# Performance work log

Hardware: AMD Instinct MI355X
Metric: run time of the kernel (lower is better)

## Reference

```python
import jax, jax.numpy as jnp
import numpy as np


def setup_inputs() -> dict:
    key = jax.random.key(0)
    ks = jax.random.split(key, 8)
    B, L, I, H, O = 512, 512, 256, 1024, 1
    def glorot(k, shape, fan_sum):
        return jax.random.uniform(k, shape, jnp.float32, -1.0, 1.0) * (6.0 / fan_sum) ** 0.5
    return {
        "X": jax.random.normal(ks[0], (B, L, I), jnp.float32),
        "W_in1": glorot(ks[1], (H, I), H + I),
        "b_in1": jnp.zeros((H, 1), jnp.float32),
        "W_rec1": glorot(ks[2], (H, H), H + H),
        "W_in2": glorot(ks[3], (H, I), H + I),
        "b_in2": jnp.zeros((H, 1), jnp.float32),
        "W_rec2": glorot(ks[4], (H, H), H + H),
        "W_out": glorot(ks[5], (O, H), O + H),
        "b_out": jnp.zeros((O, 1), jnp.float32),
    }


def reference(X, W_in1, b_in1, W_rec1, W_in2, b_in2, W_rec2, W_out, b_out):
    B, L, I = X.shape
    H = W_in1.shape[0]
    Xs = jnp.swapaxes(X, 0, 1)  # (L, B, I)
    # Precompute the input-to-hidden projections for all timesteps (parallel GEMMs).
    in1 = jnp.einsum("hi,lbi->lbh", W_in1, Xs) + b_in1[:, 0]  # (L, B, H)
    in2 = jnp.einsum("hi,lbi->lbh", W_in2, Xs) + b_in2[:, 0]  # (L, B, H)
    even = (jnp.arange(L) % 2 == 0)[:, None, None]  # (L, 1, 1) broadcast mask

    def step(carry, xs):
        z12, z1, z2 = carry  # each (B, H)
        a1, a2, ev = xs
        z1n = jnp.tanh(a1 + z12 @ W_rec1.T)
        z2n = jnp.where(ev, jnp.tanh(a2 + z2 @ W_rec2.T), z2)  # branch updates only on even l
        return (z1n + z2n, z1n, z2n), None

    z0 = jnp.zeros((B, H), X.dtype)
    (z12, z1, z2), _ = jax.lax.scan(step, (z0, z0, z0), (in1, in2, even))
    z_out = jnp.tanh(z1 @ W_out.T + b_out[:, 0])  # (B, num_outputs)
    return z_out.reshape(B, 1)
```

## Files before the change

### kernel.cpp

```cpp
#include <hip/hip_runtime.h>
#include <hip/hip_bf16.h>

typedef __attribute__((ext_vector_type(8))) short bhalf8;
typedef __attribute__((ext_vector_type(4))) float fvec4;
typedef __attribute__((ext_vector_type(4))) unsigned u32x4;

static __device__ __forceinline__ unsigned short f2bf(float f) {
  unsigned u = __builtin_bit_cast(unsigned, f);
  u = (u + 0x7fffu + ((u >> 16) & 1u)) >> 16;
  return (unsigned short)u;
}
static __device__ __forceinline__ float tanh_fast(float x) {
  x = fminf(12.f, fmaxf(-12.f, x));
  float e = __expf(2.f * x);
  return (e - 1.f) / (e + 1.f);
}
static __device__ __forceinline__ fvec4 tanh4(fvec4 v) {
  fvec4 r;
  r[0] = tanh_fast(v[0]); r[1] = tanh_fast(v[1]);
  r[2] = tanh_fast(v[2]); r[3] = tanh_fast(v[3]);
  return r;
}
static __device__ __forceinline__ bhalf8 load_w8(const float* p) {
  fvec4 a = *(const fvec4*)p;
  fvec4 b = *(const fvec4*)(p + 4);
  bhalf8 r;
  r[0] = (short)f2bf(a[0]); r[1] = (short)f2bf(a[1]);
  r[2] = (short)f2bf(a[2]); r[3] = (short)f2bf(a[3]);
  r[4] = (short)f2bf(b[0]); r[5] = (short)f2bf(b[1]);
  r[6] = (short)f2bf(b[2]); r[7] = (short)f2bf(b[3]);
  return r;
}

static __device__ __forceinline__ void st_f32_coh(float* p, float v) {
  asm volatile("global_store_dword %0, %1, off sc0 sc1" :: "v"(p), "v"(v) : "memory");
}
static __device__ __forceinline__ void st_u32_coh(unsigned* p, unsigned v) {
  asm volatile("global_store_dword %0, %1, off sc0 sc1" :: "v"(p), "v"(v) : "memory");
}
static __device__ __forceinline__ void st16_coh(void* p, u32x4 v) {
  asm volatile("global_store_dwordx4 %0, %1, off sc0 sc1" :: "v"(p), "v"(v) : "memory");
}
static __device__ __forceinline__ unsigned ld_u32_coh(const unsigned* p) {
  unsigned v;
  asm volatile("global_load_dword %0, %1, off sc0 sc1\n\ts_waitcnt vmcnt(0)"
               : "=v"(v) : "v"(p) : "memory");
  return v;
}
static __device__ __forceinline__ float ld_f32_coh(const float* p) {
  float v;
  asm volatile("global_load_dword %0, %1, off sc0 sc1\n\ts_waitcnt vmcnt(0)"
               : "=v"(v) : "v"(p) : "memory");
  return v;
}
static __device__ __forceinline__ void gll16_coh(const void* g, void* lds) {
  __builtin_amdgcn_global_load_lds(
      (const __attribute__((address_space(1))) void*)g,
      (__attribute__((address_space(3))) void*)lds, 16, 0, 0x11);
}

#define MFMA16(a, b, c) __builtin_amdgcn_mfma_f32_16x16x32_bf16((a), (b), (c), 0, 0, 0)

extern "C" __global__ void __launch_bounds__(256, 1)
alarm_rnn_persist(const float* __restrict__ X, const float* __restrict__ Win1,
                  const float* __restrict__ bin1, const float* __restrict__ Wrec1,
                  const float* __restrict__ Win2, const float* __restrict__ bin2,
                  const float* __restrict__ Wrec2, const float* __restrict__ Wout,
                  const float* __restrict__ bout, float* __restrict__ out,
                  unsigned* flags, unsigned short* gbuf0, unsigned short* gbuf1,
                  unsigned short* z2b0, unsigned short* z2b1, float* z1buf)
{
  constexpr int kL = 512, kI = 256, kH = 1024;
  extern __shared__ char smem[];

  const int tid = threadIdx.x, bid = blockIdx.x;
  const int grp = bid >> 4, memb = bid & 15;
  const int lane = tid & 63, w = tid >> 6;
  const int row16 = lane & 15, kq = lane >> 4;
  const int sw = (row16 & 7) << 4;
  const int hcol = memb * 64 + w * 16 + row16;
  const int brow0 = grp * 32;

  bhalf8 w1[32], w2[32], wi1[8], wi2[8];
  {
    const float* p1 = Wrec1 + (size_t)hcol * kH + kq * 8;
    const float* p2 = Wrec2 + (size_t)hcol * kH + kq * 8;
#pragma unroll
    for (int kk = 0; kk < 32; ++kk) {
      w1[kk] = load_w8(p1 + kk * 32);
      w2[kk] = load_w8(p2 + kk * 32);
    }
    const float* q1 = Win1 + (size_t)hcol * kI + kq * 8;
    const float* q2 = Win2 + (size_t)hcol * kI + kq * 8;
#pragma unroll
    for (int kk = 0; kk < 8; ++kk) {
      wi1[kk] = load_w8(q1 + kk * 32);
      wi2[kk] = load_w8(q2 + kk * 32);
    }
  }
  const float bv1 = bin1[hcol];
  const float bv2 = bin2[hcol];
  fvec4 z2c0 = {0.f, 0.f, 0.f, 0.f}, z2c1 = {0.f, 0.f, 0.f, 0.f};

  {
    int r = tid >> 3, q = tid & 7;
#pragma unroll
    for (int p = 0; p < 2; ++p) {
      const float* xp = X + (size_t)(brow0 + r) * (kL * kI) + (size_t)p * kI;
      fvec4 xv[8];
#pragma unroll
      for (int j = 0; j < 8; ++j) xv[j] = *(const fvec4*)(xp + q * 4 + j * 32);
#pragma unroll
      for (int j = 0; j < 8; ++j) {
        int i0 = q * 4 + j * 32;
        ushort4 pk;
        pk.x = f2bf(xv[j][0]); pk.y = f2bf(xv[j][1]);
        pk.z = f2bf(xv[j][2]); pk.w = f2bf(xv[j][3]);
        *(ushort4*)(smem + 131072 + p * 16384 + (r << 9) + ((i0 * 2) ^ ((r & 7) << 4))) = pk;
      }
    }
  }
  __syncthreads();

  for (int l = 0; l < kL; ++l) {
    const bool even = ((l & 1) == 0);
    const int e = l >> 1;

    {
      const unsigned short* zsrc = (l & 1) ? gbuf1 : gbuf0;
#pragma unroll
      for (int it = 0; it < 16; ++it) {
        int itx = (it + memb) & 15;
        int c = ((itx * 4 + w) << 6) + lane;
        int r = c >> 7, cbs = (c & 127) * 16;
        gll16_coh((const char*)zsrc + (((size_t)(brow0 + r)) << 11) + (cbs ^ ((r & 7) << 4)),
                  smem + ((itx * 4 + w) << 10));
      }
      if (even) {
        const unsigned short* z2src = (e & 1) ? z2b1 : z2b0;
#pragma unroll
        for (int it = 0; it < 16; ++it) {
          int itx = (it + memb) & 15;
          int c = ((itx * 4 + w) << 6) + lane;
          int r = c >> 7, cbs = (c & 127) * 16;
          gll16_coh((const char*)z2src + (((size_t)(brow0 + r)) << 11) + (cbs ^ ((r & 7) << 4)),
                    smem + 65536 + ((itx * 4 + w) << 10));
        }
      }
      __builtin_amdgcn_sched_barrier(0);
    }

    const char* xb = smem + 131072 + ((l & 1) << 14);
    fvec4 acc0 = {bv1, bv1, bv1, bv1}, acc1 = acc0;
#pragma unroll
    for (int kk = 0; kk < 8; ++kk) {
      int cb = kk * 64 + kq * 16;
      bhalf8 a0 = *(const bhalf8*)(xb + (row16 << 9) + (cb ^ sw));
      bhalf8 a1 = *(const bhalf8*)(xb + ((16 + row16) << 9) + (cb ^ sw));
      acc0 = MFMA16(a0, wi1[kk], acc0);
      acc1 = MFMA16(a1, wi1[kk], acc1);
    }
    fvec4 c2a0 = {bv2, bv2, bv2, bv2}, c2a1 = c2a0;
    if (even) {
#pragma unroll
      for (int kk = 0; kk < 8; ++kk) {
        int cb = kk * 64 + kq * 16;
        bhalf8 a0 = *(const bhalf8*)(xb + (row16 << 9) + (cb ^ sw));
        bhalf8 a1 = *(const bhalf8*)(xb + ((16 + row16) << 9) + (cb ^ sw));
        c2a0 = MFMA16(a0, wi2[kk], c2a0);
        c2a1 = MFMA16(a1, wi2[kk], c2a1);
      }
    }
    asm volatile("s_waitcnt vmcnt(0)" ::: "memory");
    __builtin_amdgcn_sched_barrier(0);
    __syncthreads();

#pragma unroll
    for (int kk = 0; kk < 32; ++kk) {
      int cb = kk * 64 + kq * 16;
      bhalf8 a0 = *(const bhalf8*)(smem + (row16 << 11) + (cb ^ sw));
      bhalf8 a1 = *(const bhalf8*)(smem + ((16 + row16) << 11) + (cb ^ sw));
      acc0 = MFMA16(a0, w1[kk], acc0);
      acc1 = MFMA16(a1, w1[kk], acc1);
    }
    fvec4 z1n0 = tanh4(acc0), z1n1 = tanh4(acc1);

    if (even) {
#pragma unroll
      for (int kk = 0; kk < 32; ++kk) {
        int cb = kk * 64 + kq * 16;
        bhalf8 a0 = *(const bhalf8*)(smem + 65536 + (row16 << 11) + (cb ^ sw));
        bhalf8 a1 = *(const bhalf8*)(smem + 65536 + ((16 + row16) << 11) + (cb ^ sw));
        c2a0 = MFMA16(a0, w2[kk], c2a0);
        c2a1 = MFMA16(a1, w2[kk], c2a1);
      }
      z2c0 = tanh4(c2a0);
      z2c1 = tanh4(c2a1);
    }

    __syncthreads();
    if (l < kL - 1) {
      const int colb = (w * 16 + row16) * 2;
#pragma unroll
      for (int i = 0; i < 4; ++i) {
        int r0 = kq * 4 + i, r1 = 16 + kq * 4 + i;
        *(unsigned short*)(smem + r0 * 128 + (colb ^ ((r0 & 7) << 4))) = f2bf(z1n0[i] + z2c0[i]);
        *(unsigned short*)(smem + r1 * 128 + (colb ^ ((r1 & 7) << 4))) = f2bf(z1n1[i] + z2c1[i]);
      }
      if (even) {
#pragma unroll
        for (int i = 0; i < 4; ++i) {
          int r0 = kq * 4 + i, r1 = 16 + kq * 4 + i;
          *(unsigned short*)(smem + 4096 + r0 * 128 + (colb ^ ((r0 & 7) << 4))) = f2bf(z2c0[i]);
          *(unsigned short*)(smem + 4096 + r1 * 128 + (colb ^ ((r1 & 7) << 4))) = f2bf(z2c1[i]);
        }
      }
      __syncthreads();
      {
        int r = tid >> 3, s = tid & 7;
        u32x4 v = *(const u32x4*)(smem + r * 128 + ((s * 16) ^ ((r & 7) << 4)));
        unsigned short* dst = (l & 1) ? gbuf0 : gbuf1;
        st16_coh((char*)dst + (((size_t)(brow0 + r)) << 11) + memb * 128 + s * 16, v);
        if (even) {
          u32x4 v2 = *(const u32x4*)(smem + 4096 + r * 128 + ((s * 16) ^ ((r & 7) << 4)));
          unsigned short* z2dst = (e & 1) ? z2b0 : z2b1;
          st16_coh((char*)z2dst + (((size_t)(brow0 + r)) << 11) + memb * 128 + s * 16, v2);
        }
      }
    } else {
#pragma unroll
      for (int i = 0; i < 4; ++i) {
        st_f32_coh(z1buf + (size_t)(brow0 + kq * 4 + i) * kH + hcol, z1n0[i]);
        st_f32_coh(z1buf + (size_t)(brow0 + 16 + kq * 4 + i) * kH + hcol, z1n1[i]);
      }
    }
    asm volatile("s_waitcnt vmcnt(0)" ::: "memory");
    __syncthreads();
    if (tid == 0) st_u32_coh(flags + grp * 16 + memb, (unsigned)(l + 1));

    if (l + 2 < kL) {
      const int xr = tid >> 3, xq = tid & 7;
      const float* xp = X + (size_t)(brow0 + xr) * (kL * kI) + (size_t)(l + 2) * kI;
      fvec4 xv[8];
#pragma unroll
      for (int j = 0; j < 8; ++j) xv[j] = *(const fvec4*)(xp + xq * 4 + j * 32);
#pragma unroll
      for (int j = 0; j < 8; ++j) {
        int i0 = xq * 4 + j * 32;
        ushort4 pk;
        pk.x = f2bf(xv[j][0]); pk.y = f2bf(xv[j][1]);
        pk.z = f2bf(xv[j][2]); pk.w = f2bf(xv[j][3]);
        *(ushort4*)(smem + 131072 + ((l & 1) << 14) + (xr << 9) + ((i0 * 2) ^ ((xr & 7) << 4))) = pk;
      }
    }

    {
      const unsigned tgt = (unsigned)(l + 1);
      const unsigned* fp = flags + grp * 16 + (lane & 15);
      for (;;) {
        unsigned v = (lane < 16) ? ld_u32_coh(fp) : tgt;
        bool ok = (lane >= 16) || ((lane & 15) == memb) || (v >= tgt);
        if (__all(ok)) break;
        __builtin_amdgcn_s_sleep(1);
      }
      __builtin_amdgcn_sched_barrier(0);
    }
  }

  if (memb == 0) {
    int r = tid >> 3, q = tid & 7;
    const float* zr = z1buf + (size_t)(brow0 + r) * kH;
    float s = 0.f;
    for (int h = q * 128; h < q * 128 + 128; ++h) s += ld_f32_coh(zr + h) * Wout[h];
    s += __shfl_xor(s, 1);
    s += __shfl_xor(s, 2);
    s += __shfl_xor(s, 4);
    if (q == 0) out[brow0 + r] = tanh_fast(s + bout[0]);
  }
}

extern "C" void kernel_launch(void* const* d_in, const int* in_sizes, int n_in,
                              void* d_out, int out_size, void* d_ws, size_t ws_size,
                              hipStream_t stream) {
  const float* X = (const float*)d_in[0];
  const float* Win1 = (const float*)d_in[1];
  const float* bin1 = (const float*)d_in[2];
  const float* Wrec1 = (const float*)d_in[3];
  const float* Win2 = (const float*)d_in[4];
  const float* bin2 = (const float*)d_in[5];
  const float* Wrec2 = (const float*)d_in[6];
  const float* Wout = (const float*)d_in[7];
  const float* bout = (const float*)d_in[8];
  float* out = (float*)d_out;

  char* ws = (char*)d_ws;
  unsigned* flags = (unsigned*)ws;
  unsigned short* gbuf0 = (unsigned short*)(ws + 4096);
  unsigned short* gbuf1 = (unsigned short*)(ws + 4096 + (1 << 20));
  unsigned short* z2b0 = (unsigned short*)(ws + 4096 + (2 << 20));
  unsigned short* z2b1 = (unsigned short*)(ws + 4096 + (3 << 20));
  float* z1buf = (float*)(ws + 4096 + (4 << 20));

  (void)hipMemsetAsync(flags, 0, 4096, stream);
  (void)hipMemsetAsync(gbuf0, 0, (size_t)512 * 1024 * 2, stream);
  (void)hipMemsetAsync(z2b0, 0, (size_t)512 * 1024 * 2, stream);

  (void)hipFuncSetAttribute((const void*)alarm_rnn_persist,
                            hipFuncAttributeMaxDynamicSharedMemorySize, 163840);

  alarm_rnn_persist<<<dim3(256), dim3(256), 163840, stream>>>(
      X, Win1, bin1, Wrec1, Win2, bin2, Wrec2, Wout, bout, out,
      flags, gbuf0, gbuf1, z2b0, z2b1, z1buf);
}
```

Before: 5.479 ms.

## Split recurrent GEMM across waves by K and reduce partials in LDS

Each wave now holds weight fragments for all four 16-column tiles over a quarter of the K dimension instead of one column tile over full K. A-operand fragments read from LDS are reused across four N tiles, reducing LDS read traffic per step. Partial accumulators are written to shared memory and summed across waves before bias and tanh, which adds a barrier, an LDS reduction and more live accumulator registers.

New measurement: 5.173 ms. 1.06x faster.

```diff
diff --git a/kernel.cpp b/kernel.cpp
--- a/kernel.cpp
+++ b/kernel.cpp
@@ -82,20 +82,18 @@
   const int brow0 = grp * 32;
 
   bhalf8 w1[32], w2[32], wi1[8], wi2[8];
-  {
-    const float* p1 = Wrec1 + (size_t)hcol * kH + kq * 8;
-    const float* p2 = Wrec2 + (size_t)hcol * kH + kq * 8;
-#pragma unroll
-    for (int kk = 0; kk < 32; ++kk) {
-      w1[kk] = load_w8(p1 + kk * 32);
-      w2[kk] = load_w8(p2 + kk * 32);
-    }
-    const float* q1 = Win1 + (size_t)hcol * kI + kq * 8;
-    const float* q2 = Win2 + (size_t)hcol * kI + kq * 8;
+#pragma unroll
+  for (int nt = 0; nt < 4; ++nt) {
+    const size_t c = (size_t)(memb * 64 + nt * 16 + row16);
 #pragma unroll
     for (int kk = 0; kk < 8; ++kk) {
-      wi1[kk] = load_w8(q1 + kk * 32);
-      wi2[kk] = load_w8(q2 + kk * 32);
+      w1[nt * 8 + kk] = load_w8(Wrec1 + c * kH + w * 256 + kk * 32 + kq * 8);
+      w2[nt * 8 + kk] = load_w8(Wrec2 + c * kH + w * 256 + kk * 32 + kq * 8);
+    }
+#pragma unroll
+    for (int k2 = 0; k2 < 2; ++k2) {
+      wi1[nt * 2 + k2] = load_w8(Win1 + c * kI + w * 64 + k2 * 32 + kq * 8);
+      wi2[nt * 2 + k2] = load_w8(Win2 + c * kI + w * 64 + k2 * 32 + kq * 8);
     }
   }
   const float bv1 = bin1[hcol];
@@ -151,24 +149,25 @@
     }
 
     const char* xb = smem + 131072 + ((l & 1) << 14);
-    fvec4 acc0 = {bv1, bv1, bv1, bv1}, acc1 = acc0;
-#pragma unroll
-    for (int kk = 0; kk < 8; ++kk) {
-      int cb = kk * 64 + kq * 16;
-      bhalf8 a0 = *(const bhalf8*)(xb + (row16 << 9) + (cb ^ sw));
-      bhalf8 a1 = *(const bhalf8*)(xb + ((16 + row16) << 9) + (cb ^ sw));
-      acc0 = MFMA16(a0, wi1[kk], acc0);
-      acc1 = MFMA16(a1, wi1[kk], acc1);
-    }
-    fvec4 c2a0 = {bv2, bv2, bv2, bv2}, c2a1 = c2a0;
-    if (even) {
-#pragma unroll
-      for (int kk = 0; kk < 8; ++kk) {
-        int cb = kk * 64 + kq * 16;
-        bhalf8 a0 = *(const bhalf8*)(xb + (row16 << 9) + (cb ^ sw));
-        bhalf8 a1 = *(const bhalf8*)(xb + ((16 + row16) << 9) + (cb ^ sw));
-        c2a0 = MFMA16(a0, wi2[kk], c2a0);
-        c2a1 = MFMA16(a1, wi2[kk], c2a1);
+    fvec4 acc[8], c2a[8];
+#pragma unroll
+    for (int t = 0; t < 8; ++t) { acc[t] = {0.f, 0.f, 0.f, 0.f}; c2a[t] = {0.f, 0.f, 0.f, 0.f}; }
+#pragma unroll
+    for (int k2 = 0; k2 < 2; ++k2) {
+      int cbx = (w * 2 + k2) * 64 + kq * 16;
+      bhalf8 xa0 = *(const bhalf8*)(xb + (row16 << 9) + (cbx ^ sw));
+      bhalf8 xa1 = *(const bhalf8*)(xb + ((16 + row16) << 9) + (cbx ^ sw));
+#pragma unroll
+      for (int nt = 0; nt < 4; ++nt) {
+        acc[nt * 2] = MFMA16(xa0, wi1[nt * 2 + k2], acc[nt * 2]);
+        acc[nt * 2 + 1] = MFMA16(xa1, wi1[nt * 2 + k2], acc[nt * 2 + 1]);
+      }
+      if (even) {
+#pragma unroll
+        for (int nt = 0; nt < 4; ++nt) {
+          c2a[nt * 2] = MFMA16(xa0, wi2[nt * 2 + k2], c2a[nt * 2]);
+          c2a[nt * 2 + 1] = MFMA16(xa1, wi2[nt * 2 + k2], c2a[nt * 2 + 1]);
+        }
       }
     }
     asm volatile("s_waitcnt vmcnt(0)" ::: "memory");
@@ -176,53 +175,103 @@
     __syncthreads();
 
 #pragma unroll
-    for (int kk = 0; kk < 32; ++kk) {
-      int cb = kk * 64 + kq * 16;
+    for (int kk = 0; kk < 8; ++kk) {
+      int cb = (w * 8 + kk) * 64 + kq * 16;
       bhalf8 a0 = *(const bhalf8*)(smem + (row16 << 11) + (cb ^ sw));
       bhalf8 a1 = *(const bhalf8*)(smem + ((16 + row16) << 11) + (cb ^ sw));
-      acc0 = MFMA16(a0, w1[kk], acc0);
-      acc1 = MFMA16(a1, w1[kk], acc1);
-    }
-    fvec4 z1n0 = tanh4(acc0), z1n1 = tanh4(acc1);
-
+#pragma unroll
+      for (int nt = 0; nt < 4; ++nt) {
+        acc[nt * 2] = MFMA16(a0, w1[nt * 8 + kk], acc[nt * 2]);
+        acc[nt * 2 + 1] = MFMA16(a1, w1[nt * 8 + kk], acc[nt * 2 + 1]);
+      }
+    }
     if (even) {
 #pragma unroll
-      for (int kk = 0; kk < 32; ++kk) {
-        int cb = kk * 64 + kq * 16;
+      for (int kk = 0; kk < 8; ++kk) {
+        int cb = (w * 8 + kk) * 64 + kq * 16;
         bhalf8 a0 = *(const bhalf8*)(smem + 65536 + (row16 << 11) + (cb ^ sw));
         bhalf8 a1 = *(const bhalf8*)(smem + 65536 + ((16 + row16) << 11) + (cb ^ sw));
-        c2a0 = MFMA16(a0, w2[kk], c2a0);
-        c2a1 = MFMA16(a1, w2[kk], c2a1);
-      }
-      z2c0 = tanh4(c2a0);
-      z2c1 = tanh4(c2a1);
+#pragma unroll
+        for (int nt = 0; nt < 4; ++nt) {
+          c2a[nt * 2] = MFMA16(a0, w2[nt * 8 + kk], c2a[nt * 2]);
+          c2a[nt * 2 + 1] = MFMA16(a1, w2[nt * 8 + kk], c2a[nt * 2 + 1]);
+        }
+      }
     }
 
     __syncthreads();
+#pragma unroll
+    for (int nt = 0; nt < 4; ++nt)
+#pragma unroll
+      for (int mt = 0; mt < 2; ++mt) {
+        int base = (((nt * 2 + mt) * 4 + w) << 10);
+        fvec4 v = acc[nt * 2 + mt];
+#pragma unroll
+        for (int i = 0; i < 4; ++i)
+          *(float*)(smem + base + (((kq * 4 + i) * 16 + row16) << 2)) = v[i];
+        if (even) {
+          fvec4 v2 = c2a[nt * 2 + mt];
+#pragma unroll
+          for (int i = 0; i < 4; ++i)
+            *(float*)(smem + 32768 + base + (((kq * 4 + i) * 16 + row16) << 2)) = v2[i];
+        }
+      }
+    __syncthreads();
+
+    fvec4 s0 = {0.f, 0.f, 0.f, 0.f}, s1 = s0;
+#pragma unroll
+    for (int ws = 0; ws < 4; ++ws) {
+      int b0 = (((w * 2 + 0) * 4 + ws) << 10), b1 = (((w * 2 + 1) * 4 + ws) << 10);
+#pragma unroll
+      for (int i = 0; i < 4; ++i) {
+        s0[i] += *(const float*)(smem + b0 + (((kq * 4 + i) * 16 + row16) << 2));
+        s1[i] += *(const float*)(smem + b1 + (((kq * 4 + i) * 16 + row16) << 2));
+      }
+    }
+#pragma unroll
+    for (int i = 0; i < 4; ++i) { s0[i] += bv1; s1[i] += bv1; }
+    fvec4 z1n0 = tanh4(s0), z1n1 = tanh4(s1);
+    if (even) {
+      fvec4 t0 = {0.f, 0.f, 0.f, 0.f}, t1 = t0;
+#pragma unroll
+      for (int ws = 0; ws < 4; ++ws) {
+        int b0 = 32768 + (((w * 2 + 0) * 4 + ws) << 10), b1 = 32768 + (((w * 2 + 1) * 4 + ws) << 10);
+#pragma unroll
+        for (int i = 0; i < 4; ++i) {
+          t0[i] += *(const float*)(smem + b0 + (((kq * 4 + i) * 16 + row16) << 2));
+          t1[i] += *(const float*)(smem + b1 + (((kq * 4 + i) * 16 + row16) << 2));
+        }
+      }
+#pragma unroll
+      for (int i = 0; i < 4; ++i) { t0[i] += bv2; t1[i] += bv2; }
+      z2c0 = tanh4(t0);
+      z2c1 = tanh4(t1);
+    }
+
     if (l < kL - 1) {
       const int colb = (w * 16 + row16) * 2;
 #pragma unroll
       for (int i = 0; i < 4; ++i) {
         int r0 = kq * 4 + i, r1 = 16 + kq * 4 + i;
-        *(unsigned short*)(smem + r0 * 128 + (colb ^ ((r0 & 7) << 4))) = f2bf(z1n0[i] + z2c0[i]);
-        *(unsigned short*)(smem + r1 * 128 + (colb ^ ((r1 & 7) << 4))) = f2bf(z1n1[i] + z2c1[i]);
+        *(unsigned short*)(smem + 65536 + r0 * 128 + (colb ^ ((r0 & 7) << 4))) = f2bf(z1n0[i] + z2c0[i]);
+        *(unsigned short*)(smem + 65536 + r1 * 128 + (colb ^ ((r1 & 7) << 4))) = f2bf(z1n1[i] + z2c1[i]);
       }
       if (even) {
 #pragma unroll
         for (int i = 0; i < 4; ++i) {
           int r0 = kq * 4 + i, r1 = 16 + kq * 4 + i;
-          *(unsigned short*)(smem + 4096 + r0 * 128 + (colb ^ ((r0 & 7) << 4))) = f2bf(z2c0[i]);
-          *(unsigned short*)(smem + 4096 + r1 * 128 + (colb ^ ((r1 & 7) << 4))) = f2bf(z2c1[i]);
+          *(unsigned short*)(smem + 69632 + r0 * 128 + (colb ^ ((r0 & 7) << 4))) = f2bf(z2c0[i]);
+          *(unsigned short*)(smem + 69632 + r1 * 128 + (colb ^ ((r1 & 7) << 4))) = f2bf(z2c1[i]);
         }
       }
       __syncthreads();
       {
         int r = tid >> 3, s = tid & 7;
-        u32x4 v = *(const u32x4*)(smem + r * 128 + ((s * 16) ^ ((r & 7) << 4)));
+        u32x4 v = *(const u32x4*)(smem + 65536 + r * 128 + ((s * 16) ^ ((r & 7) << 4)));
         unsigned short* dst = (l & 1) ? gbuf0 : gbuf1;
         st16_coh((char*)dst + (((size_t)(brow0 + r)) << 11) + memb * 128 + s * 16, v);
         if (even) {
-          u32x4 v2 = *(const u32x4*)(smem + 4096 + r * 128 + ((s * 16) ^ ((r & 7) << 4)));
+          u32x4 v2 = *(const u32x4*)(smem + 69632 + r * 128 + ((s * 16) ^ ((r & 7) << 4)));
           unsigned short* z2dst = (e & 1) ? z2b0 : z2b1;
           st16_coh((char*)z2dst + (((size_t)(brow0 + r)) << 11) + memb * 128 + s * 16, v2);
         }
```
